# Kernel optimization log

Measured on AMD Instinct MI355X. Metric: run time of the kernel, lower is better.

## Reference

```python
import jax, jax.numpy as jnp
import numpy as np
import math

D_MODEL = 1024
N_HEAD = 16
D_K = 64
D_V = 64
EPS = 1e-6


def setup_inputs() -> dict:
    key = jax.random.key(0)
    ks = jax.random.split(key, 10)
    B, S = 4, 2048
    inp = {
        'x_queries': jax.random.normal(ks[0], (B, S, D_MODEL), jnp.float32),
        'x_keys': jax.random.normal(ks[1], (B, S, D_MODEL), jnp.float32),
        'x_values': jax.random.normal(ks[2], (B, S, D_MODEL), jnp.float32),
        'mask': jax.random.randint(ks[3], (B, S, S), 0, 2, jnp.int32),
        # Linear(d_model, n_head*d_k, bias=False) weights stored as [in, out]
        'w_q': jax.random.normal(ks[4], (D_MODEL, N_HEAD * D_K), jnp.float32) * np.sqrt(2.0 / (D_MODEL + D_K)),
        'w_k': jax.random.normal(ks[5], (D_MODEL, N_HEAD * D_K), jnp.float32) * np.sqrt(2.0 / (D_MODEL + D_K)),
        'w_v': jax.random.normal(ks[6], (D_MODEL, N_HEAD * D_V), jnp.float32) * np.sqrt(2.0 / (D_MODEL + D_V)),
        'w_0': jax.random.normal(ks[7], (N_HEAD * D_V, D_MODEL), jnp.float32) * np.sqrt(2.0 / (N_HEAD * D_V + D_MODEL)),
        'gamma': jnp.ones((D_MODEL,), jnp.float32),
        'beta': jnp.zeros((D_MODEL,), jnp.float32),
    }
    return inp


def _layer_norm(x, gamma, beta, eps=EPS):
    # Matches the torch module: std with Bessel correction, eps added to std.
    mean = jnp.mean(x, axis=-1, keepdims=True)
    std = jnp.std(x, axis=-1, keepdims=True, ddof=1)
    return gamma * (x - mean) / (std + eps) + beta


def reference(x_queries, x_keys, x_values, mask, w_q, w_k, w_v, w_0, gamma, beta):
    B, Lq, _ = x_queries.shape
    residual = x_queries
    # Projections -> [B, L, H, D]
    Q = (x_queries @ w_q).reshape(B, Lq, N_HEAD, D_K)
    K = (x_keys @ w_k).reshape(B, x_keys.shape[1], N_HEAD, D_K)
    V = (x_values @ w_v).reshape(B, x_values.shape[1], N_HEAD, D_V)
    # Scaled dot-product attention (scores materialized as in the original bmm path)
    scores = jnp.einsum('bqhd,bkhd->bhqk', Q, K) / math.sqrt(D_K)
    # NOTE: original masked_fill uses eps (not -inf) where mask == 0
    scores = jnp.where(mask[:, None, :, :] == 0, EPS, scores)
    attn = jax.nn.softmax(scores, axis=-1)
    out = jnp.einsum('bhqk,bkhd->bqhd', attn, V).reshape(B, Lq, N_HEAD * D_V)
    out = out @ w_0
    return _layer_norm(out + residual, gamma, beta)
```

## Files before the change

kernel.cpp:

```cpp
#include <hip/hip_runtime.h>
#include <hip/hip_bf16.h>

#define DM 1024
#define NH 16
#define DK 64
#define BB 4
#define SS 2048
#define EPSV 1e-6f
#define NE ((size_t)BB * SS * DM)
#define MM ((size_t)DM * DM)

typedef __attribute__((ext_vector_type(8))) short short8;
typedef __attribute__((ext_vector_type(4))) float f32x4;

__device__ inline unsigned short f2bf(float x) {
  unsigned int u = __builtin_bit_cast(unsigned int, x);
  u += 0x7FFF + ((u >> 16) & 1);
  return (unsigned short)(u >> 16);
}
__device__ inline ushort4 f2bf4(float4 v) {
  ushort4 r;
  r.x = f2bf(v.x); r.y = f2bf(v.y); r.z = f2bf(v.z); r.w = f2bf(v.w);
  return r;
}

__device__ inline void gl_lds16(const unsigned short* g, unsigned short* l) {
  __builtin_amdgcn_global_load_lds((const __attribute__((address_space(1))) void*)g,
                                   (__attribute__((address_space(3))) void*)l, 16, 0, 0);
}

__global__ __launch_bounds__(256) void cvt_x_k(const float* __restrict__ xq,
                                               const float* __restrict__ xk,
                                               const float* __restrict__ xv,
                                               unsigned short* __restrict__ oq,
                                               unsigned short* __restrict__ ok,
                                               unsigned short* __restrict__ ov) {
  const size_t NF4 = NE / 4;
  size_t g = (size_t)blockIdx.x * 256 + threadIdx.x;
  int t = (int)(g / NF4);
  size_t i = g - (size_t)t * NF4;
  const float* s = (t == 0) ? xq : (t == 1) ? xk : xv;
  unsigned short* d = (t == 0) ? oq : (t == 1) ? ok : ov;
  float4 v = ((const float4*)s)[i];
  ((ushort4*)d)[i] = f2bf4(v);
}

__global__ __launch_bounds__(256) void cvt_wT_k(const float* __restrict__ w0,
                                                const float* __restrict__ w1,
                                                const float* __restrict__ w2,
                                                const float* __restrict__ w3,
                                                unsigned short* __restrict__ o0,
                                                unsigned short* __restrict__ o1,
                                                unsigned short* __restrict__ o2,
                                                unsigned short* __restrict__ o3) {
  __shared__ float t[32][33];
  int z = blockIdx.z;
  const float* w = (z == 0) ? w0 : (z == 1) ? w1 : (z == 2) ? w2 : w3;
  unsigned short* o = (z == 0) ? o0 : (z == 1) ? o1 : (z == 2) ? o2 : o3;
  int n0 = blockIdx.x * 32, k0 = blockIdx.y * 32;
  int tx = threadIdx.x & 31, ty = threadIdx.x >> 5;
#pragma unroll
  for (int s = 0; s < 4; ++s) t[ty + s * 8][tx] = w[(size_t)(k0 + ty + s * 8) * DM + n0 + tx];
  __syncthreads();
#pragma unroll
  for (int s = 0; s < 4; ++s)
    o[(size_t)(n0 + ty + s * 8) * DM + k0 + tx] = f2bf(t[tx][ty + s * 8]);
}

__global__ __launch_bounds__(256) void maskbits_k(const int* __restrict__ mask,
                                                  unsigned long long* __restrict__ bm) {
  const int total = BB * SS * (SS / 64);
  int lane = threadIdx.x & 63;
  int wid = (blockIdx.x * 256 + threadIdx.x) >> 6;
  int nw = (gridDim.x * 256) >> 6;
  for (int w = wid; w < total; w += nw) {
    int v = mask[(size_t)w * 64 + lane];
    unsigned long long bal = __ballot(v != 0);
    if (lane == 0) bm[w] = bal;
  }
}

template <bool BF16OUT>
__global__ __launch_bounds__(256) void gemm_lds_k(const unsigned short* __restrict__ Abase,
                                                  const unsigned short* __restrict__ WTbase,
                                                  void* __restrict__ Cv, int M, int N, int K,
                                                  size_t zA, size_t zW, size_t zC) {
  __shared__ __align__(16) unsigned short As[128 * 32];
  __shared__ __align__(16) unsigned short Bs[128 * 32];
  const unsigned short* A = Abase + (size_t)blockIdx.z * zA;
  const unsigned short* WT = WTbase + (size_t)blockIdx.z * zW;
  int bm = blockIdx.y * 128, bn = blockIdx.x * 128;
  int tid = threadIdx.x, lane = tid & 63, w = tid >> 6;
  int quad = lane >> 4, c = lane & 15, wx = w & 1, wy = w >> 1;

  f32x4 acc[4][4];
#pragma unroll
  for (int mt = 0; mt < 4; ++mt)
#pragma unroll
    for (int nt = 0; nt < 4; ++nt)
#pragma unroll
      for (int r = 0; r < 4; ++r) acc[mt][nt][r] = 0.f;

  int srow = lane >> 2, scol = (lane & 3) * 8;
  const unsigned short* Ag = A + (size_t)(bm + w * 32 + srow) * K + scol;
  const unsigned short* Bg = WT + (size_t)(bn + w * 32 + srow) * K + scol;
  unsigned short* Al = &As[w * 32 * 32];
  unsigned short* Bl = &Bs[w * 32 * 32];

  for (int k0 = 0; k0 < K; k0 += 32) {
    gl_lds16(Ag + k0, Al);
    gl_lds16(Ag + (size_t)16 * K + k0, Al + 16 * 32);
    gl_lds16(Bg + k0, Bl);
    gl_lds16(Bg + (size_t)16 * K + k0, Bl + 16 * 32);
    __syncthreads();
    short8 af[4], bf[4];
#pragma unroll
    for (int mt = 0; mt < 4; ++mt) af[mt] = *(const short8*)&As[(wy * 64 + mt * 16 + c) * 32 + quad * 8];
#pragma unroll
    for (int nt = 0; nt < 4; ++nt) bf[nt] = *(const short8*)&Bs[(wx * 64 + nt * 16 + c) * 32 + quad * 8];
#pragma unroll
    for (int mt = 0; mt < 4; ++mt)
#pragma unroll
      for (int nt = 0; nt < 4; ++nt)
        acc[mt][nt] = __builtin_amdgcn_mfma_f32_16x16x32_bf16(af[mt], bf[nt], acc[mt][nt], 0, 0, 0);
    __syncthreads();
  }
#pragma unroll
  for (int mt = 0; mt < 4; ++mt)
#pragma unroll
    for (int nt = 0; nt < 4; ++nt)
#pragma unroll
      for (int r = 0; r < 4; ++r) {
        size_t idx = (size_t)blockIdx.z * zC +
                     (size_t)(bm + wy * 64 + mt * 16 + quad * 4 + r) * N + bn + wx * 64 + nt * 16 + c;
        if (BF16OUT)
          ((unsigned short*)Cv)[idx] = f2bf(acc[mt][nt][r]);
        else
          ((float*)Cv)[idx] = acc[mt][nt][r];
      }
}

__global__ __launch_bounds__(256) void attn_mfma_k(const unsigned short* __restrict__ Q,
                                                   const unsigned short* __restrict__ Kg,
                                                   const unsigned short* __restrict__ V,
                                                   const unsigned long long* __restrict__ bm,
                                                   unsigned short* __restrict__ O) {
  __shared__ __align__(16) unsigned short Ks[64 * 72];
  __shared__ __align__(16) unsigned short VB[64 * 64];
  __shared__ __align__(16) unsigned short Ps[64 * 72];
  int b = blockIdx.z, h = blockIdx.y, q0 = blockIdx.x * 64;
  int tid = threadIdx.x, lane = tid & 63, w = tid >> 6;
  int quad = lane >> 4, c = lane & 15;

  short8 qf[2];
  {
    const unsigned short* qp = Q + ((size_t)b * SS + q0 + w * 16 + c) * DM + h * DK + quad * 8;
    qf[0] = *(const short8*)qp;
    qf[1] = *(const short8*)(qp + 32);
  }

  float lpart[4] = {0.f, 0.f, 0.f, 0.f};
  f32x4 accO[4];
#pragma unroll
  for (int dt = 0; dt < 4; ++dt)
#pragma unroll
    for (int r = 0; r < 4; ++r) accO[dt][r] = 0.f;

  int krow = tid >> 3, kd = (tid & 7) * 8;
  int vd = tid & 63, vkb = (tid >> 6) * 8;
  int vdt = vd >> 4, vc = vd & 15;

  for (int kt = 0; kt < SS / 64; ++kt) {
    int k0 = kt * 64;
#pragma unroll
    for (int pass = 0; pass < 2; ++pass) {
      int kr = krow + pass * 32;
      short8 kv = *(const short8*)&Kg[((size_t)b * SS + k0 + kr) * DM + h * DK + kd];
      *(short8*)&Ks[kr * 72 + kd] = kv;
    }
#pragma unroll
    for (int s = 0; s < 2; ++s) {
      int kb = vkb + s * 32;
      const unsigned short* vp = &V[((size_t)b * SS + k0 + kb) * DM + h * DK + vd];
      union { short8 v; unsigned short u[8]; } pk;
#pragma unroll
      for (int j = 0; j < 8; ++j) pk.u[j] = vp[(size_t)j * DM];
      *(short8*)&VB[(((kb >> 5) * 4 + vdt) * 4 + ((kb >> 3) & 3)) * 128 + vc * 8] = pk.v;
    }
    __syncthreads();

    f32x4 sacc[4];
#pragma unroll
    for (int nt = 0; nt < 4; ++nt)
#pragma unroll
      for (int r = 0; r < 4; ++r) sacc[nt][r] = 0.f;
#pragma unroll
    for (int dkt = 0; dkt < 2; ++dkt)
#pragma unroll
      for (int nt = 0; nt < 4; ++nt) {
        short8 kfrag = *(const short8*)&Ks[(nt * 16 + c) * 72 + dkt * 32 + quad * 8];
        sacc[nt] = __builtin_amdgcn_mfma_f32_16x16x32_bf16(qf[dkt], kfrag, sacc[nt], 0, 0, 0);
      }

#pragma unroll
    for (int r = 0; r < 4; ++r) {
      int q = q0 + w * 16 + quad * 4 + r;
      unsigned long long mw = bm[((size_t)b * SS + q) * (SS / 64) + kt];
      int prow = (w * 16 + quad * 4 + r) * 72;
      float rs = 0.f;
#pragma unroll
      for (int nt = 0; nt < 4; ++nt) {
        float p = ((mw >> (nt * 16 + c)) & 1ull) ? __expf(sacc[nt][r] * 0.125f) : 1.0f;
        rs += p;
        Ps[prow + nt * 16 + c] = f2bf(p);
      }
      lpart[r] += rs;
    }

#pragma unroll
    for (int pkt = 0; pkt < 2; ++pkt) {
      short8 pf = *(const short8*)&Ps[(w * 16 + c) * 72 + pkt * 32 + quad * 8];
#pragma unroll
      for (int dt = 0; dt < 4; ++dt) {
        short8 vf = *(const short8*)&VB[((pkt * 4 + dt) * 4 + quad) * 128 + c * 8];
        accO[dt] = __builtin_amdgcn_mfma_f32_16x16x32_bf16(pf, vf, accO[dt], 0, 0, 0);
      }
    }
    __syncthreads();
  }

  float inv[4];
#pragma unroll
  for (int r = 0; r < 4; ++r) {
    float l = lpart[r];
    l += __shfl_xor(l, 1);
    l += __shfl_xor(l, 2);
    l += __shfl_xor(l, 4);
    l += __shfl_xor(l, 8);
    inv[r] = 1.f / l;
  }
#pragma unroll
  for (int dt = 0; dt < 4; ++dt)
#pragma unroll
    for (int r = 0; r < 4; ++r) {
      int q = q0 + w * 16 + quad * 4 + r;
      O[((size_t)b * SS + q) * DM + h * DK + dt * 16 + c] = f2bf(accO[dt][r] * inv[r]);
    }
}

__global__ __launch_bounds__(256) void ln_k(const float* __restrict__ P,
                                            const float* __restrict__ X,
                                            const float* __restrict__ gamma,
                                            const float* __restrict__ beta,
                                            float* __restrict__ out) {
  __shared__ float sm[4];
  int row = blockIdx.x, tid = threadIdx.x, w = tid >> 6;
  float4 p = ((const float4*)(P + (size_t)row * DM))[tid];
  float4 x = ((const float4*)(X + (size_t)row * DM))[tid];
  float4 v = make_float4(p.x + x.x, p.y + x.y, p.z + x.z, p.w + x.w);
  float s = (v.x + v.y) + (v.z + v.w);
#pragma unroll
  for (int off = 1; off < 64; off <<= 1) s += __shfl_xor(s, off);
  if ((tid & 63) == 0) sm[w] = s;
  __syncthreads();
  float mean = (sm[0] + sm[1] + sm[2] + sm[3]) * (1.f / DM);
  __syncthreads();
  float dx = v.x - mean, dy = v.y - mean, dz = v.z - mean, dw = v.w - mean;
  float s2 = (dx * dx + dy * dy) + (dz * dz + dw * dw);
#pragma unroll
  for (int off = 1; off < 64; off <<= 1) s2 += __shfl_xor(s2, off);
  if ((tid & 63) == 0) sm[w] = s2;
  __syncthreads();
  float var = (sm[0] + sm[1] + sm[2] + sm[3]) * (1.f / (DM - 1));
  float inv = 1.f / (sqrtf(var) + EPSV);
  float4 g = ((const float4*)gamma)[tid];
  float4 be = ((const float4*)beta)[tid];
  float4 y = make_float4(g.x * dx * inv + be.x, g.y * dy * inv + be.y,
                         g.z * dz * inv + be.z, g.w * dw * inv + be.w);
  ((float4*)(out + (size_t)row * DM))[tid] = y;
}

extern "C" void kernel_launch(void* const* d_in, const int* in_sizes, int n_in,
                              void* d_out, int out_size, void* d_ws, size_t ws_size,
                              hipStream_t stream) {
  const float* xq = (const float*)d_in[0];
  const float* xk = (const float*)d_in[1];
  const float* xv = (const float*)d_in[2];
  const int* mask = (const int*)d_in[3];
  const float* wq = (const float*)d_in[4];
  const float* wk = (const float*)d_in[5];
  const float* wv = (const float*)d_in[6];
  const float* w0 = (const float*)d_in[7];
  const float* gamma = (const float*)d_in[8];
  const float* beta = (const float*)d_in[9];
  float* out = (float*)d_out;

  unsigned short* xqb = (unsigned short*)d_ws;
  unsigned short* xkb = xqb + NE;
  unsigned short* xvb = xkb + NE;
  unsigned short* wTq = xvb + NE;
  unsigned short* wTk = wTq + MM;
  unsigned short* wTv = wTk + MM;
  unsigned short* wT0 = wTv + MM;
  unsigned short* Qb = wT0 + MM;
  unsigned short* Kb = Qb + NE;
  unsigned short* Vb = Kb + NE;
  unsigned short* AOb = Vb + NE;
  float* P = (float*)Qb;
  unsigned long long* bm = (unsigned long long*)d_out;

  const int M = BB * SS;
  cvt_x_k<<<(unsigned)(3 * (NE / 4) / 256), 256, 0, stream>>>(xq, xk, xv, xqb, xkb, xvb);
  cvt_wT_k<<<dim3(32, 32, 4), 256, 0, stream>>>(wq, wk, wv, w0, wTq, wTk, wTv, wT0);
  maskbits_k<<<256, 256, 0, stream>>>(mask, bm);
  gemm_lds_k<true><<<dim3(DM / 128, M / 128, 3), 256, 0, stream>>>(
      xqb, wTq, Qb, M, DM, DM, NE, MM, NE);
  attn_mfma_k<<<dim3(SS / 64, NH, BB), 256, 0, stream>>>(Qb, Kb, Vb, bm, AOb);
  gemm_lds_k<false><<<dim3(DM / 128, M / 128, 1), 256, 0, stream>>>(
      AOb, wT0, P, M, DM, DM, 0, 0, 0);
  ln_k<<<M, 256, 0, stream>>>(P, xq, gamma, beta, out);
}
```

Baseline: 605.6 us.

## Keep attention probabilities in registers via transposed QK MFMA and exp2 prescaling

New measurement: 563.3 us. 1.08x faster.

```diff
diff --git a/kernel.cpp b/kernel.cpp
--- a/kernel.cpp
+++ b/kernel.cpp
@@ -1,5 +1,6 @@
 #include <hip/hip_runtime.h>
 #include <hip/hip_bf16.h>
+#include <math.h>
 
 #define DM 1024
 #define NH 16
@@ -9,6 +10,7 @@
 #define EPSV 1e-6f
 #define NE ((size_t)BB * SS * DM)
 #define MM ((size_t)DM * DM)
+#define QSCALE 0.18033688011112042f
 
 typedef __attribute__((ext_vector_type(8))) short short8;
 typedef __attribute__((ext_vector_type(4))) float f32x4;
@@ -21,6 +23,20 @@
 __device__ inline ushort4 f2bf4(float4 v) {
   ushort4 r;
   r.x = f2bf(v.x); r.y = f2bf(v.y); r.z = f2bf(v.z); r.w = f2bf(v.w);
+  return r;
+}
+
+__device__ inline float fexp2(float x) {
+#if __has_builtin(__builtin_amdgcn_exp2f)
+  return __builtin_amdgcn_exp2f(x);
+#else
+  return exp2f(x);
+#endif
+}
+
+__device__ inline unsigned cvtpk_bf16(float a, float b) {
+  unsigned r;
+  asm("v_cvt_pk_bf16_f32 %0, %1, %2" : "=v"(r) : "v"(a), "v"(b));
   return r;
 }
 
@@ -57,6 +73,7 @@
   int z = blockIdx.z;
   const float* w = (z == 0) ? w0 : (z == 1) ? w1 : (z == 2) ? w2 : w3;
   unsigned short* o = (z == 0) ? o0 : (z == 1) ? o1 : (z == 2) ? o2 : o3;
+  float sc = (z == 0) ? QSCALE : 1.0f;
   int n0 = blockIdx.x * 32, k0 = blockIdx.y * 32;
   int tx = threadIdx.x & 31, ty = threadIdx.x >> 5;
 #pragma unroll
@@ -64,7 +81,7 @@
   __syncthreads();
 #pragma unroll
   for (int s = 0; s < 4; ++s)
-    o[(size_t)(n0 + ty + s * 8) * DM + k0 + tx] = f2bf(t[tx][ty + s * 8]);
+    o[(size_t)(n0 + ty + s * 8) * DM + k0 + tx] = f2bf(t[tx][ty + s * 8] * sc);
 }
 
 __global__ __launch_bounds__(256) void maskbits_k(const int* __restrict__ mask,
@@ -147,7 +164,6 @@
                                                    unsigned short* __restrict__ O) {
   __shared__ __align__(16) unsigned short Ks[64 * 72];
   __shared__ __align__(16) unsigned short VB[64 * 64];
-  __shared__ __align__(16) unsigned short Ps[64 * 72];
   int b = blockIdx.z, h = blockIdx.y, q0 = blockIdx.x * 64;
   int tid = threadIdx.x, lane = tid & 63, w = tid >> 6;
   int quad = lane >> 4, c = lane & 15;
@@ -158,8 +174,10 @@
     qf[0] = *(const short8*)qp;
     qf[1] = *(const short8*)(qp + 32);
   }
-
-  float lpart[4] = {0.f, 0.f, 0.f, 0.f};
+  const unsigned long long* bp = bm + ((size_t)b * SS + q0 + w * 16 + c) * (SS / 64);
+  const int shq = quad * 4;
+
+  float lsum = 0.f;
   f32x4 accO[4];
 #pragma unroll
   for (int dt = 0; dt < 4; ++dt)
@@ -167,8 +185,7 @@
     for (int r = 0; r < 4; ++r) accO[dt][r] = 0.f;
 
   int krow = tid >> 3, kd = (tid & 7) * 8;
-  int vd = tid & 63, vkb = (tid >> 6) * 8;
-  int vdt = vd >> 4, vc = vd & 15;
+  int vd = tid & 63, vdt = vd >> 4, vc = vd & 15;
 
   for (int kt = 0; kt < SS / 64; ++kt) {
     int k0 = kt * 64;
@@ -178,14 +195,14 @@
       short8 kv = *(const short8*)&Kg[((size_t)b * SS + k0 + kr) * DM + h * DK + kd];
       *(short8*)&Ks[kr * 72 + kd] = kv;
     }
+    const unsigned short* vtile = &V[((size_t)b * SS + k0) * DM + h * DK + vd];
 #pragma unroll
     for (int s = 0; s < 2; ++s) {
-      int kb = vkb + s * 32;
-      const unsigned short* vp = &V[((size_t)b * SS + k0 + kb) * DM + h * DK + vd];
       union { short8 v; unsigned short u[8]; } pk;
 #pragma unroll
-      for (int j = 0; j < 8; ++j) pk.u[j] = vp[(size_t)j * DM];
-      *(short8*)&VB[(((kb >> 5) * 4 + vdt) * 4 + ((kb >> 3) & 3)) * 128 + vc * 8] = pk.v;
+      for (int j = 0; j < 8; ++j)
+        pk.u[j] = vtile[(size_t)(s * 32 + (j >> 2) * 16 + w * 4 + (j & 3)) * DM];
+      *(short8*)&VB[((s * 4 + vdt) * 4 + w) * 128 + vc * 8] = pk.v;
     }
     __syncthreads();
 
@@ -199,46 +216,50 @@
 #pragma unroll
       for (int nt = 0; nt < 4; ++nt) {
         short8 kfrag = *(const short8*)&Ks[(nt * 16 + c) * 72 + dkt * 32 + quad * 8];
-        sacc[nt] = __builtin_amdgcn_mfma_f32_16x16x32_bf16(qf[dkt], kfrag, sacc[nt], 0, 0, 0);
+        sacc[nt] = __builtin_amdgcn_mfma_f32_16x16x32_bf16(kfrag, qf[dkt], sacc[nt], 0, 0, 0);
       }
 
-#pragma unroll
-    for (int r = 0; r < 4; ++r) {
-      int q = q0 + w * 16 + quad * 4 + r;
-      unsigned long long mw = bm[((size_t)b * SS + q) * (SS / 64) + kt];
-      int prow = (w * 16 + quad * 4 + r) * 72;
-      float rs = 0.f;
-#pragma unroll
-      for (int nt = 0; nt < 4; ++nt) {
-        float p = ((mw >> (nt * 16 + c)) & 1ull) ? __expf(sacc[nt][r] * 0.125f) : 1.0f;
-        rs += p;
-        Ps[prow + nt * 16 + c] = f2bf(p);
+    unsigned long long mwv = bp[kt];
+    unsigned long long msh = mwv >> shq;
+    unsigned mlo = (unsigned)msh, mhi = (unsigned)(msh >> 32);
+    unsigned padw[8];
+#pragma unroll
+    for (int nt = 0; nt < 4; ++nt) {
+      unsigned msel = (nt & 2) ? mhi : mlo;
+      const int bse = (nt & 1) * 16;
+      float pv[4];
+#pragma unroll
+      for (int r = 0; r < 4; ++r) {
+        float ex = fexp2(sacc[nt][r]);
+        pv[r] = ((msel >> (bse + r)) & 1u) ? ex : 1.0f;
+        lsum += pv[r];
       }
-      lpart[r] += rs;
+      padw[nt * 2] = cvtpk_bf16(pv[0], pv[1]);
+      padw[nt * 2 + 1] = cvtpk_bf16(pv[2], pv[3]);
     }
 
 #pragma unroll
     for (int pkt = 0; pkt < 2; ++pkt) {
-      short8 pf = *(const short8*)&Ps[(w * 16 + c) * 72 + pkt * 32 + quad * 8];
+      union { unsigned u[4]; short8 s8; } pa;
+      pa.u[0] = padw[pkt * 4 + 0];
+      pa.u[1] = padw[pkt * 4 + 1];
+      pa.u[2] = padw[pkt * 4 + 2];
+      pa.u[3] = padw[pkt * 4 + 3];
 #pragma unroll
       for (int dt = 0; dt < 4; ++dt) {
         short8 vf = *(const short8*)&VB[((pkt * 4 + dt) * 4 + quad) * 128 + c * 8];
-        accO[dt] = __builtin_amdgcn_mfma_f32_16x16x32_bf16(pf, vf, accO[dt], 0, 0, 0);
+        accO[dt] = __builtin_amdgcn_mfma_f32_16x16x32_bf16(pa.s8, vf, accO[dt], 0, 0, 0);
       }
     }
     __syncthreads();
   }
 
+  float l = lsum;
+  l += __shfl_xor(l, 16);
+  l += __shfl_xor(l, 32);
   float inv[4];
 #pragma unroll
-  for (int r = 0; r < 4; ++r) {
-    float l = lpart[r];
-    l += __shfl_xor(l, 1);
-    l += __shfl_xor(l, 2);
-    l += __shfl_xor(l, 4);
-    l += __shfl_xor(l, 8);
-    inv[r] = 1.f / l;
-  }
+  for (int r = 0; r < 4; ++r) inv[r] = 1.f / __shfl(l, quad * 4 + r);
 #pragma unroll
   for (int dt = 0; dt < 4; ++dt)
 #pragma unroll
```
